# Performance work log

Hardware: AMD Instinct MI355X
Metric: run time of the kernel (lower is better)

Reference implementation:

```python
import jax, jax.numpy as jnp
import numpy as np
from jax import lax

N_CODES = 4880
T = 4096
VISIT_DIM = 512
HDIM = 512


def setup_inputs() -> dict:
    key = jax.random.key(0)
    ks = jax.random.split(key, 8)
    s_in = 1.0 / np.sqrt(HDIM)
    return {
        "H": jax.random.uniform(ks[0], (N_CODES, T), dtype=jnp.float32),
        "TE": jnp.zeros((1,), dtype=jnp.float32),
        "X_emb": jax.random.normal(ks[1], (N_CODES, VISIT_DIM), dtype=jnp.float32) * 0.02,
        "W_ih": jax.random.uniform(ks[2], (3 * HDIM, VISIT_DIM), minval=-s_in, maxval=s_in, dtype=jnp.float32),
        "W_hh": jax.random.uniform(ks[3], (3 * HDIM, HDIM), minval=-s_in, maxval=s_in, dtype=jnp.float32),
        "b_ih": jax.random.uniform(ks[4], (3 * HDIM,), minval=-s_in, maxval=s_in, dtype=jnp.float32),
        "b_hh": jax.random.uniform(ks[5], (3 * HDIM,), minval=-s_in, maxval=s_in, dtype=jnp.float32),
        "w_att": jax.random.uniform(ks[6], (1, HDIM), minval=-s_in, maxval=s_in, dtype=jnp.float32),
    }


def _gru_scan(visit_emb, W_ih, W_hh, b_ih, b_hh):
    # Precompute input projections for all timesteps: [T, 3H]
    gi = visit_emb @ W_ih.T + b_ih
    H = W_hh.shape[1]

    def step(h, gi_t):
        gh = h @ W_hh.T + b_hh  # [3H]
        i_r, i_z, i_n = gi_t[:H], gi_t[H:2 * H], gi_t[2 * H:]
        h_r, h_z, h_n = gh[:H], gh[H:2 * H], gh[2 * H:]
        r = jax.nn.sigmoid(i_r + h_r)
        z = jax.nn.sigmoid(i_z + h_z)
        n = jnp.tanh(i_n + r * h_n)
        h_new = (1.0 - z) * n + z * h
        return h_new, h_new

    h0 = jnp.zeros((H,), dtype=visit_emb.dtype)
    _, hs = lax.scan(step, h0, gi)
    return hs  # [T, H]


def reference(H, TE, X_emb, W_ih, W_hh, b_ih, b_hh, w_att):
    # visit embeddings: [T, visit_dim]
    visit_emb = H.T @ X_emb
    # GRU over the visit sequence (unbatched): [T, hdim]
    hidden_states = _gru_scan(visit_emb, W_ih, W_hh, b_ih, b_hh)
    # attention logits [T] -> softmax over visits
    logits = hidden_states @ w_att[0]
    alpha = jax.nn.softmax(logits)
    # diag(alpha) @ hidden summed over dim 0 == weighted sum over visits
    h = jnp.sum(alpha[:, None] * hidden_states, axis=0)  # [hdim]
    return h
```

## Files before the change

### kernel.cpp

```cpp
#include <hip/hip_runtime.h>

#define T_STEPS 4096
#define HD 512
#define G3HD 1536
#define NCODES 4880
#define NWG 16
#define SENT 0xFFFFFFFFu

typedef __attribute__((ext_vector_type(2))) float v2f;
typedef __attribute__((ext_vector_type(4))) unsigned uint4v;

__global__ __launch_bounds__(256) void gemm1_kernel(const float* __restrict__ H,
                                                    const float* __restrict__ X,
                                                    float* __restrict__ C) {
  __shared__ float As[16][68];
  __shared__ float Bs[16][68];
  const int m0 = blockIdx.x * 64;
  const int n0 = blockIdx.y * 64;
  const int tid = threadIdx.x;
  const int lk = tid >> 4;
  const int lm = (tid & 15) << 2;
  const int tm = (tid & 15) << 2;
  const int tn = (tid >> 4) << 2;
  float acc[4][4] = {};
  for (int k0 = 0; k0 < NCODES; k0 += 16) {
    float4 av = *(const float4*)(H + (size_t)(k0 + lk) * T_STEPS + m0 + lm);
    float4 bv = *(const float4*)(X + (size_t)(k0 + lk) * HD + n0 + lm);
    __syncthreads();
    *(float4*)(&As[lk][lm]) = av;
    *(float4*)(&Bs[lk][lm]) = bv;
    __syncthreads();
#pragma unroll
    for (int kk = 0; kk < 16; ++kk) {
      float4 a = *(const float4*)(&As[kk][tm]);
      float4 b = *(const float4*)(&Bs[kk][tn]);
      float ar[4] = {a.x, a.y, a.z, a.w};
      float br[4] = {b.x, b.y, b.z, b.w};
#pragma unroll
      for (int i = 0; i < 4; ++i)
#pragma unroll
        for (int j = 0; j < 4; ++j) acc[i][j] += ar[i] * br[j];
    }
  }
#pragma unroll
  for (int i = 0; i < 4; ++i) {
    float4 o = make_float4(acc[i][0], acc[i][1], acc[i][2], acc[i][3]);
    *(float4*)(C + (size_t)(m0 + tm + i) * HD + n0 + tn) = o;
  }
}

__global__ __launch_bounds__(256) void gemm2_kernel(const float* __restrict__ A,
                                                    const float* __restrict__ B,
                                                    const float* __restrict__ bias,
                                                    float* __restrict__ Cout) {
  __shared__ float As[16][68];
  __shared__ float Bs[16][68];
  const int m0 = blockIdx.x * 64;
  const int n0 = blockIdx.y * 64;
  const int tid = threadIdx.x;
  const int lr = tid >> 2;
  const int lkq = (tid & 3) << 2;
  const int tm = (tid & 15) << 2;
  const int tn = (tid >> 4) << 2;
  float acc[4][4] = {};
  for (int k0 = 0; k0 < HD; k0 += 16) {
    float4 av = *(const float4*)(A + (size_t)(m0 + lr) * HD + k0 + lkq);
    float4 bv = *(const float4*)(B + (size_t)(n0 + lr) * HD + k0 + lkq);
    __syncthreads();
    As[lkq + 0][lr] = av.x; As[lkq + 1][lr] = av.y;
    As[lkq + 2][lr] = av.z; As[lkq + 3][lr] = av.w;
    Bs[lkq + 0][lr] = bv.x; Bs[lkq + 1][lr] = bv.y;
    Bs[lkq + 2][lr] = bv.z; Bs[lkq + 3][lr] = bv.w;
    __syncthreads();
#pragma unroll
    for (int kk = 0; kk < 16; ++kk) {
      float4 a = *(const float4*)(&As[kk][tm]);
      float4 b = *(const float4*)(&Bs[kk][tn]);
      float ar[4] = {a.x, a.y, a.z, a.w};
      float br[4] = {b.x, b.y, b.z, b.w};
#pragma unroll
      for (int i = 0; i < 4; ++i)
#pragma unroll
        for (int j = 0; j < 4; ++j) acc[i][j] += ar[i] * br[j];
    }
  }
  const float b0 = bias[n0 + tn + 0];
  const float b1 = bias[n0 + tn + 1];
  const float b2 = bias[n0 + tn + 2];
  const float b3 = bias[n0 + tn + 3];
#pragma unroll
  for (int i = 0; i < 4; ++i) {
    float4 o = make_float4(acc[i][0] + b0, acc[i][1] + b1, acc[i][2] + b2, acc[i][3] + b3);
    *(float4*)(Cout + (size_t)(m0 + tm + i) * G3HD + n0 + tn) = o;
  }
}

__global__ __launch_bounds__(512, 1) void scan_kernel(const float* __restrict__ gi,
                                                      const float* __restrict__ W_hh,
                                                      const float* __restrict__ b_hh,
                                                      float* __restrict__ hs,
                                                      int* __restrict__ ctrl) {
  __shared__ int s_role;
  __shared__ __align__(16) float gibuf[2][64][96];
  __shared__ __align__(16) float hT[HD];
  __shared__ float part[8][3][32];
  const int tid = threadIdx.x;

  if (tid == 0) {
    int xcd;
    asm volatile("s_getreg_b32 %0, hwreg(HW_REG_XCC_ID)" : "=s"(xcd));
    int role = -1;
    const int slot = atomicAdd(&ctrl[xcd], 1);
    if (slot < NWG) {
      if (slot == NWG - 1) atomicCAS(&ctrl[8], -1, xcd);
      int wnr;
      while ((wnr = __hip_atomic_load(&ctrl[8], __ATOMIC_RELAXED,
                                      __HIP_MEMORY_SCOPE_AGENT)) < 0) {
        __builtin_amdgcn_s_sleep(16);
      }
      if (wnr == xcd) role = slot;
    }
    s_role = role;
  }
  __syncthreads();
  const int g = s_role;
  if (g < 0) return;

  const int w = tid >> 6;
  const int lane = tid & 63;
  const int e2 = lane & 31;
  const int q = lane >> 5;
  const int k0 = w * 64 + q * 32;

  v2f w2[3][16];
#pragma unroll
  for (int r = 0; r < 3; ++r) {
    const v2f* wp = (const v2f*)(W_hh + (size_t)(r * HD + g * 32 + e2) * HD + k0);
#pragma unroll
    for (int j = 0; j < 16; ++j) w2[r][j] = wp[j];
  }
#pragma unroll
  for (int r = 0; r < 3; ++r)
#pragma unroll
    for (int j = 0; j < 16; ++j) asm volatile("" : "+v"(w2[r][j]));

  float bh_r = 0.f, bh_z = 0.f, bh_n = 0.f, hprev = 0.f;
  if (tid < 32) {
    const int ej = g * 32 + tid;
    bh_r = b_hh[ej];
    bh_z = b_hh[HD + ej];
    bh_n = b_hh[2 * HD + ej];
  }

  unsigned* hs_u = (unsigned*)hs;

  uint4v st[3];
#pragma unroll
  for (int j = 0; j < 3; ++j) {
    const int c = tid + 512 * j, row = c / 24, seg = c % 24;
    st[j] = *(const uint4v*)(gi + (size_t)row * G3HD + (seg >> 3) * HD + g * 32 + (seg & 7) * 4);
  }
#pragma unroll
  for (int j = 0; j < 3; ++j) {
    const int c = tid + 512 * j, row = c / 24, seg = c % 24;
    *(uint4v*)&gibuf[0][row][(seg >> 3) * 32 + (seg & 7) * 4] = st[j];
  }
  __syncthreads();

  for (int t = 0; t < T_STEPS; ++t) {
    const int cb = (t >> 6) & 1;
    const int ts = t & 63;

    if (t == 0) {
      hT[tid] = 0.f;
    } else {
      const unsigned* hp = hs_u + (size_t)(t - 1) * HD + tid;
      unsigned v = __hip_atomic_load(hp, __ATOMIC_RELAXED, __HIP_MEMORY_SCOPE_AGENT);
      while (v == SENT)
        v = __hip_atomic_load(hp, __ATOMIC_RELAXED, __HIP_MEMORY_SCOPE_AGENT);
      hT[tid] = __uint_as_float(v);
    }
    __syncthreads();

    const v2f* hv = (const v2f*)&hT[k0];
    v2f h2[16];
#pragma unroll
    for (int m = 0; m < 16; ++m) h2[m] = hv[m];
    v2f a0 = (v2f)(0.f), a1 = (v2f)(0.f), a2 = (v2f)(0.f);
#pragma unroll
    for (int m = 0; m < 16; ++m) {
      a0 = __builtin_elementwise_fma(w2[0][m], h2[m], a0);
      a1 = __builtin_elementwise_fma(w2[1][m], h2[m], a1);
      a2 = __builtin_elementwise_fma(w2[2][m], h2[m], a2);
    }
    float s0 = a0.x + a0.y;
    float s1 = a1.x + a1.y;
    float s2 = a2.x + a2.y;
    s0 += __shfl_xor(s0, 32);
    s1 += __shfl_xor(s1, 32);
    s2 += __shfl_xor(s2, 32);
    if (q == 0) {
      part[w][0][e2] = s0;
      part[w][1][e2] = s1;
      part[w][2][e2] = s2;
    }

    if (ts == 0 && t + 64 < T_STEPS) {
#pragma unroll
      for (int j = 0; j < 3; ++j) {
        const int c = tid + 512 * j, row = c / 24, seg = c % 24;
        st[j] = *(const uint4v*)(gi + (size_t)(t + 64 + row) * G3HD + (seg >> 3) * HD +
                                 g * 32 + (seg & 7) * 4);
      }
    }
    if (ts == 1 && t + 63 < T_STEPS) {
#pragma unroll
      for (int j = 0; j < 3; ++j) {
        const int c = tid + 512 * j, row = c / 24, seg = c % 24;
        *(uint4v*)&gibuf[cb ^ 1][row][(seg >> 3) * 32 + (seg & 7) * 4] = st[j];
      }
    }
    __syncthreads();

    if (tid < 32) {
      float xr = 0.f, xz = 0.f, xn = 0.f;
#pragma unroll
      for (int ww = 0; ww < 8; ++ww) {
        xr += part[ww][0][tid];
        xz += part[ww][1][tid];
        xn += part[ww][2][tid];
      }
      const float gir = gibuf[cb][ts][tid];
      const float giz = gibuf[cb][ts][32 + tid];
      const float gin = gibuf[cb][ts][64 + tid];
      xr += gir + bh_r;
      xz += giz + bh_z;
      const float ghn = xn + bh_n;
      const float rr = __builtin_amdgcn_rcpf(1.f + __expf(-xr));
      const float zz = __builtin_amdgcn_rcpf(1.f + __expf(-xz));
      const float y = gin + rr * ghn;
      const float nn = 1.f - 2.f * __builtin_amdgcn_rcpf(__expf(2.f * y) + 1.f);
      const float hnew = nn + zz * (hprev - nn);
      __hip_atomic_store(hs_u + (size_t)t * HD + g * 32 + tid, __float_as_uint(hnew),
                         __ATOMIC_RELAXED, __HIP_MEMORY_SCOPE_AGENT);
      hprev = hnew;
    }
  }
}

__global__ __launch_bounds__(256) void logits_kernel(const float* __restrict__ hs,
                                                     const float* __restrict__ w_att,
                                                     float* __restrict__ logits) {
  const int tid = threadIdx.x;
  const int r = blockIdx.x * 32 + (tid >> 3);
  const int c0 = (tid & 7) * 64;
  const float4* hp = (const float4*)(hs + (size_t)r * HD + c0);
  const float4* wp = (const float4*)(w_att + c0);
  float acc = 0.f;
#pragma unroll
  for (int i = 0; i < 16; ++i) {
    float4 h4 = hp[i], w4 = wp[i];
    acc += h4.x * w4.x + h4.y * w4.y + h4.z * w4.z + h4.w * w4.w;
  }
  acc += __shfl_xor(acc, 1);
  acc += __shfl_xor(acc, 2);
  acc += __shfl_xor(acc, 4);
  if ((tid & 7) == 0) logits[r] = acc;
}

__global__ __launch_bounds__(256) void softmax_kernel(const float* __restrict__ logits,
                                                      float* __restrict__ alpha,
                                                      float* __restrict__ out) {
  __shared__ float tmp[4];
  const int tid = threadIdx.x;
  float l[16];
  float m = -1e30f;
#pragma unroll
  for (int i = 0; i < 16; ++i) {
    l[i] = logits[i * 256 + tid];
    m = fmaxf(m, l[i]);
  }
#pragma unroll
  for (int o = 32; o > 0; o >>= 1) m = fmaxf(m, __shfl_xor(m, o));
  if ((tid & 63) == 0) tmp[tid >> 6] = m;
  __syncthreads();
  m = fmaxf(fmaxf(tmp[0], tmp[1]), fmaxf(tmp[2], tmp[3]));
  __syncthreads();
  float e[16];
  float s = 0.f;
#pragma unroll
  for (int i = 0; i < 16; ++i) {
    e[i] = expf(l[i] - m);
    s += e[i];
  }
#pragma unroll
  for (int o = 32; o > 0; o >>= 1) s += __shfl_xor(s, o);
  if ((tid & 63) == 0) tmp[tid >> 6] = s;
  __syncthreads();
  s = tmp[0] + tmp[1] + tmp[2] + tmp[3];
  const float inv = 1.f / s;
#pragma unroll
  for (int i = 0; i < 16; ++i) alpha[i * 256 + tid] = e[i] * inv;
  out[tid] = 0.f;
  out[256 + tid] = 0.f;
}

__global__ __launch_bounds__(256) void wsum_kernel(const float* __restrict__ alpha,
                                                   const float* __restrict__ hs,
                                                   float* __restrict__ out) {
  const int tid = threadIdx.x;
  const int jblk = (blockIdx.x & 1) * 256;
  const int tc = blockIdx.x >> 1;
  float acc = 0.f;
  for (int tt = 0; tt < 64; ++tt) {
    const int t = tc * 64 + tt;
    acc += alpha[t] * hs[(size_t)t * HD + jblk + tid];
  }
  atomicAdd(&out[jblk + tid], acc);
}

extern "C" void kernel_launch(void* const* d_in, const int* in_sizes, int n_in,
                              void* d_out, int out_size, void* d_ws, size_t ws_size,
                              hipStream_t stream) {
  const float* H     = (const float*)d_in[0];
  const float* X_emb = (const float*)d_in[2];
  const float* W_ih  = (const float*)d_in[3];
  const float* W_hh  = (const float*)d_in[4];
  const float* b_ih  = (const float*)d_in[5];
  const float* b_hh  = (const float*)d_in[6];
  const float* w_att = (const float*)d_in[7];
  float* out = (float*)d_out;

  char* ws = (char*)d_ws;
  float* visit  = (float*)(ws + 0);
  float* gi     = (float*)(ws + 8388608);
  float* hs     = (float*)(ws + 33554432);
  float* logits = (float*)(ws + 41943040);
  float* alpha  = (float*)(ws + 41959424);
  int*   ctrl   = (int*)(ws + 41975808);

  hipMemsetAsync(hs, 0xFF, (size_t)T_STEPS * HD * sizeof(float), stream);
  hipMemsetAsync(ctrl, 0, 8 * sizeof(int), stream);
  hipMemsetAsync(ctrl + 8, 0xFF, sizeof(int), stream);

  gemm1_kernel<<<dim3(64, 8), 256, 0, stream>>>(H, X_emb, visit);
  gemm2_kernel<<<dim3(64, 24), 256, 0, stream>>>(visit, W_ih, b_ih, gi);
  scan_kernel<<<256, 512, 0, stream>>>(gi, W_hh, b_hh, hs, ctrl);
  logits_kernel<<<128, 256, 0, stream>>>(hs, w_att, logits);
  softmax_kernel<<<1, 256, 0, stream>>>(logits, alpha, out);
  wsum_kernel<<<128, 256, 0, stream>>>(alpha, hs, out);
}
```

Measured before the change: 5.558 ms.

## Remap GRU scan threads so reductions stay in-wave, drop one barrier per step

Changes the scan kernel's work split so each wave owns 4 output elements and 16 lanes split the K dimension of each. The dot products are reduced with in-wave xor shuffles, which removes the shared-memory partial buffer and the second __syncthreads per timestep. The h vector is double-buffered in LDS so the next step's write cannot race with reads, and a rotated access pattern is used to avoid bank conflicts. Gate math now runs on 32 lanes spread over 8 waves instead of one wave, at the cost of extra shuffle steps.

```diff
diff --git a/kernel.cpp b/kernel.cpp
--- a/kernel.cpp
+++ b/kernel.cpp
@@ -102,8 +102,7 @@
                                                       int* __restrict__ ctrl) {
   __shared__ int s_role;
   __shared__ __align__(16) float gibuf[2][64][96];
-  __shared__ __align__(16) float hT[HD];
-  __shared__ float part[8][3][32];
+  __shared__ __align__(16) float hT[2][HD];
   const int tid = threadIdx.x;
 
   if (tid == 0) {
@@ -128,120 +127,111 @@
 
   const int w = tid >> 6;
   const int lane = tid & 63;
-  const int e2 = lane & 31;
-  const int q = lane >> 5;
-  const int k0 = w * 64 + q * 32;
+  const int kk = lane & 15;
+  const int j = lane >> 4;
+  const int eg = g * 32 + w * 4 + j;
 
   v2f w2[3][16];
 #pragma unroll
   for (int r = 0; r < 3; ++r) {
-    const v2f* wp = (const v2f*)(W_hh + (size_t)(r * HD + g * 32 + e2) * HD + k0);
-#pragma unroll
-    for (int j = 0; j < 16; ++j) w2[r][j] = wp[j];
+    const v2f* wp = (const v2f*)(W_hh + (size_t)(r * HD + eg) * HD + kk * 32);
+#pragma unroll
+    for (int s = 0; s < 16; ++s) w2[r][s] = wp[(s + kk) & 15];
   }
 #pragma unroll
   for (int r = 0; r < 3; ++r)
 #pragma unroll
-    for (int j = 0; j < 16; ++j) asm volatile("" : "+v"(w2[r][j]));
-
+    for (int s = 0; s < 16; ++s) asm volatile("" : "+v"(w2[r][s]));
+
+  const bool is_gate = (kk == 0);
   float bh_r = 0.f, bh_z = 0.f, bh_n = 0.f, hprev = 0.f;
-  if (tid < 32) {
-    const int ej = g * 32 + tid;
-    bh_r = b_hh[ej];
-    bh_z = b_hh[HD + ej];
-    bh_n = b_hh[2 * HD + ej];
+  if (is_gate) {
+    bh_r = b_hh[eg];
+    bh_z = b_hh[HD + eg];
+    bh_n = b_hh[2 * HD + eg];
   }
 
   unsigned* hs_u = (unsigned*)hs;
 
   uint4v st[3];
 #pragma unroll
-  for (int j = 0; j < 3; ++j) {
-    const int c = tid + 512 * j, row = c / 24, seg = c % 24;
-    st[j] = *(const uint4v*)(gi + (size_t)row * G3HD + (seg >> 3) * HD + g * 32 + (seg & 7) * 4);
-  }
-#pragma unroll
-  for (int j = 0; j < 3; ++j) {
-    const int c = tid + 512 * j, row = c / 24, seg = c % 24;
-    *(uint4v*)&gibuf[0][row][(seg >> 3) * 32 + (seg & 7) * 4] = st[j];
+  for (int jj = 0; jj < 3; ++jj) {
+    const int c = tid + 512 * jj, row = c / 24, seg = c % 24;
+    st[jj] = *(const uint4v*)(gi + (size_t)row * G3HD + (seg >> 3) * HD + g * 32 + (seg & 7) * 4);
+  }
+#pragma unroll
+  for (int jj = 0; jj < 3; ++jj) {
+    const int c = tid + 512 * jj, row = c / 24, seg = c % 24;
+    *(uint4v*)&gibuf[0][row][(seg >> 3) * 32 + (seg & 7) * 4] = st[jj];
   }
   __syncthreads();
 
   for (int t = 0; t < T_STEPS; ++t) {
+    const int pb = t & 1;
     const int cb = (t >> 6) & 1;
     const int ts = t & 63;
 
     if (t == 0) {
-      hT[tid] = 0.f;
+      hT[0][tid] = 0.f;
     } else {
       const unsigned* hp = hs_u + (size_t)(t - 1) * HD + tid;
       unsigned v = __hip_atomic_load(hp, __ATOMIC_RELAXED, __HIP_MEMORY_SCOPE_AGENT);
       while (v == SENT)
         v = __hip_atomic_load(hp, __ATOMIC_RELAXED, __HIP_MEMORY_SCOPE_AGENT);
-      hT[tid] = __uint_as_float(v);
-    }
-    __syncthreads();
-
-    const v2f* hv = (const v2f*)&hT[k0];
+      hT[pb][tid] = __uint_as_float(v);
+    }
+
+    if (ts == 0 && t + 64 < T_STEPS) {
+#pragma unroll
+      for (int jj = 0; jj < 3; ++jj) {
+        const int c = tid + 512 * jj, row = c / 24, seg = c % 24;
+        st[jj] = *(const uint4v*)(gi + (size_t)(t + 64 + row) * G3HD + (seg >> 3) * HD +
+                                 g * 32 + (seg & 7) * 4);
+      }
+    }
+    __syncthreads();
+
+    if (ts == 1 && t + 63 < T_STEPS) {
+#pragma unroll
+      for (int jj = 0; jj < 3; ++jj) {
+        const int c = tid + 512 * jj, row = c / 24, seg = c % 24;
+        *(uint4v*)&gibuf[cb ^ 1][row][(seg >> 3) * 32 + (seg & 7) * 4] = st[jj];
+      }
+    }
+
+    const v2f* hv = (const v2f*)&hT[pb][kk * 32];
     v2f h2[16];
 #pragma unroll
-    for (int m = 0; m < 16; ++m) h2[m] = hv[m];
+    for (int s = 0; s < 16; ++s) h2[s] = hv[(s + kk) & 15];
     v2f a0 = (v2f)(0.f), a1 = (v2f)(0.f), a2 = (v2f)(0.f);
 #pragma unroll
-    for (int m = 0; m < 16; ++m) {
-      a0 = __builtin_elementwise_fma(w2[0][m], h2[m], a0);
-      a1 = __builtin_elementwise_fma(w2[1][m], h2[m], a1);
-      a2 = __builtin_elementwise_fma(w2[2][m], h2[m], a2);
+    for (int s = 0; s < 16; ++s) {
+      a0 = __builtin_elementwise_fma(w2[0][s], h2[s], a0);
+      a1 = __builtin_elementwise_fma(w2[1][s], h2[s], a1);
+      a2 = __builtin_elementwise_fma(w2[2][s], h2[s], a2);
     }
     float s0 = a0.x + a0.y;
     float s1 = a1.x + a1.y;
     float s2 = a2.x + a2.y;
-    s0 += __shfl_xor(s0, 32);
-    s1 += __shfl_xor(s1, 32);
-    s2 += __shfl_xor(s2, 32);
-    if (q == 0) {
-      part[w][0][e2] = s0;
-      part[w][1][e2] = s1;
-      part[w][2][e2] = s2;
-    }
-
-    if (ts == 0 && t + 64 < T_STEPS) {
-#pragma unroll
-      for (int j = 0; j < 3; ++j) {
-        const int c = tid + 512 * j, row = c / 24, seg = c % 24;
-        st[j] = *(const uint4v*)(gi + (size_t)(t + 64 + row) * G3HD + (seg >> 3) * HD +
-                                 g * 32 + (seg & 7) * 4);
-      }
-    }
-    if (ts == 1 && t + 63 < T_STEPS) {
-#pragma unroll
-      for (int j = 0; j < 3; ++j) {
-        const int c = tid + 512 * j, row = c / 24, seg = c % 24;
-        *(uint4v*)&gibuf[cb ^ 1][row][(seg >> 3) * 32 + (seg & 7) * 4] = st[j];
-      }
-    }
-    __syncthreads();
-
-    if (tid < 32) {
-      float xr = 0.f, xz = 0.f, xn = 0.f;
-#pragma unroll
-      for (int ww = 0; ww < 8; ++ww) {
-        xr += part[ww][0][tid];
-        xz += part[ww][1][tid];
-        xn += part[ww][2][tid];
-      }
-      const float gir = gibuf[cb][ts][tid];
-      const float giz = gibuf[cb][ts][32 + tid];
-      const float gin = gibuf[cb][ts][64 + tid];
-      xr += gir + bh_r;
-      xz += giz + bh_z;
-      const float ghn = xn + bh_n;
+#pragma unroll
+    for (int mask = 1; mask <= 8; mask <<= 1) {
+      s0 += __shfl_xor(s0, mask);
+      s1 += __shfl_xor(s1, mask);
+      s2 += __shfl_xor(s2, mask);
+    }
+
+    if (is_gate) {
+      const int el = w * 4 + j;
+      float xr = s0 + gibuf[cb][ts][el] + bh_r;
+      float xz = s1 + gibuf[cb][ts][32 + el] + bh_z;
+      const float ghn = s2 + bh_n;
+      const float gin = gibuf[cb][ts][64 + el];
       const float rr = __builtin_amdgcn_rcpf(1.f + __expf(-xr));
       const float zz = __builtin_amdgcn_rcpf(1.f + __expf(-xz));
       const float y = gin + rr * ghn;
       const float nn = 1.f - 2.f * __builtin_amdgcn_rcpf(__expf(2.f * y) + 1.f);
       const float hnew = nn + zz * (hprev - nn);
-      __hip_atomic_store(hs_u + (size_t)t * HD + g * 32 + tid, __float_as_uint(hnew),
+      __hip_atomic_store(hs_u + (size_t)t * HD + eg, __float_as_uint(hnew),
                          __ATOMIC_RELAXED, __HIP_MEMORY_SCOPE_AGENT);
       hprev = hnew;
     }
```

Measured after the change: 8.669 ms. 56.0% more time.

## Poll previous hidden state directly into registers, dropping the per-step LDS barrier

Applied to the files above, without the earlier changes.

Each half-wave now spin-loads its own 32-element slice of the previous hidden state from global memory with vectorized sc1 loads straight into registers. This removes the shared hT staging buffer and one __syncthreads per timestep. The partial-sum buffer is double-buffered by step parity so the single remaining barrier still keeps reads and writes separate. In exchange, polling traffic per step rises (each lane reads 128 bytes instead of 4) and correctness now depends on the inline-asm cache-bypass semantics.

```diff
diff --git a/kernel.cpp b/kernel.cpp
--- a/kernel.cpp
+++ b/kernel.cpp
@@ -102,8 +102,7 @@
                                                       int* __restrict__ ctrl) {
   __shared__ int s_role;
   __shared__ __align__(16) float gibuf[2][64][96];
-  __shared__ __align__(16) float hT[HD];
-  __shared__ float part[8][3][32];
+  __shared__ float part[2][8][3][32];
   const int tid = threadIdx.x;
 
   if (tid == 0) {
@@ -131,6 +130,7 @@
   const int e2 = lane & 31;
   const int q = lane >> 5;
   const int k0 = w * 64 + q * 32;
+  const int c = 2 * w + q;
 
   v2f w2[3][16];
 #pragma unroll
@@ -157,35 +157,71 @@
   uint4v st[3];
 #pragma unroll
   for (int j = 0; j < 3; ++j) {
-    const int c = tid + 512 * j, row = c / 24, seg = c % 24;
+    const int cc = tid + 512 * j, row = cc / 24, seg = cc % 24;
     st[j] = *(const uint4v*)(gi + (size_t)row * G3HD + (seg >> 3) * HD + g * 32 + (seg & 7) * 4);
   }
 #pragma unroll
   for (int j = 0; j < 3; ++j) {
-    const int c = tid + 512 * j, row = c / 24, seg = c % 24;
+    const int cc = tid + 512 * j, row = cc / 24, seg = cc % 24;
     *(uint4v*)&gibuf[0][row][(seg >> 3) * 32 + (seg & 7) * 4] = st[j];
   }
   __syncthreads();
 
   for (int t = 0; t < T_STEPS; ++t) {
+    const int pb = t & 1;
     const int cb = (t >> 6) & 1;
     const int ts = t & 63;
 
+    v2f h2[16];
     if (t == 0) {
-      hT[tid] = 0.f;
+#pragma unroll
+      for (int m = 0; m < 16; ++m) h2[m] = (v2f)(0.f);
     } else {
-      const unsigned* hp = hs_u + (size_t)(t - 1) * HD + tid;
-      unsigned v = __hip_atomic_load(hp, __ATOMIC_RELAXED, __HIP_MEMORY_SCOPE_AGENT);
-      while (v == SENT)
-        v = __hip_atomic_load(hp, __ATOMIC_RELAXED, __HIP_MEMORY_SCOPE_AGENT);
-      hT[tid] = __uint_as_float(v);
-    }
-    __syncthreads();
-
-    const v2f* hv = (const v2f*)&hT[k0];
-    v2f h2[16];
-#pragma unroll
-    for (int m = 0; m < 16; ++m) h2[m] = hv[m];
+      const unsigned* hp = hs_u + (size_t)(t - 1) * HD + c * 32;
+      uint4v b0, b1, b2, b3, b4, b5, b6, b7;
+      bool ok;
+      do {
+        asm volatile(
+            "global_load_dwordx4 %0, %8, off sc1\n\t"
+            "global_load_dwordx4 %1, %8, off offset:16 sc1\n\t"
+            "global_load_dwordx4 %2, %8, off offset:32 sc1\n\t"
+            "global_load_dwordx4 %3, %8, off offset:48 sc1\n\t"
+            "global_load_dwordx4 %4, %8, off offset:64 sc1\n\t"
+            "global_load_dwordx4 %5, %8, off offset:80 sc1\n\t"
+            "global_load_dwordx4 %6, %8, off offset:96 sc1\n\t"
+            "global_load_dwordx4 %7, %8, off offset:112 sc1\n\t"
+            "s_waitcnt vmcnt(0)"
+            : "=&v"(b0), "=&v"(b1), "=&v"(b2), "=&v"(b3),
+              "=&v"(b4), "=&v"(b5), "=&v"(b6), "=&v"(b7)
+            : "v"(hp)
+            : "memory");
+        ok = (b0.x != SENT) & (b0.y != SENT) & (b0.z != SENT) & (b0.w != SENT) &
+             (b1.x != SENT) & (b1.y != SENT) & (b1.z != SENT) & (b1.w != SENT) &
+             (b2.x != SENT) & (b2.y != SENT) & (b2.z != SENT) & (b2.w != SENT) &
+             (b3.x != SENT) & (b3.y != SENT) & (b3.z != SENT) & (b3.w != SENT) &
+             (b4.x != SENT) & (b4.y != SENT) & (b4.z != SENT) & (b4.w != SENT) &
+             (b5.x != SENT) & (b5.y != SENT) & (b5.z != SENT) & (b5.w != SENT) &
+             (b6.x != SENT) & (b6.y != SENT) & (b6.z != SENT) & (b6.w != SENT) &
+             (b7.x != SENT) & (b7.y != SENT) & (b7.z != SENT) & (b7.w != SENT);
+      } while (!ok);
+      h2[0].x  = __uint_as_float(b0.x); h2[0].y  = __uint_as_float(b0.y);
+      h2[1].x  = __uint_as_float(b0.z); h2[1].y  = __uint_as_float(b0.w);
+      h2[2].x  = __uint_as_float(b1.x); h2[2].y  = __uint_as_float(b1.y);
+      h2[3].x  = __uint_as_float(b1.z); h2[3].y  = __uint_as_float(b1.w);
+      h2[4].x  = __uint_as_float(b2.x); h2[4].y  = __uint_as_float(b2.y);
+      h2[5].x  = __uint_as_float(b2.z); h2[5].y  = __uint_as_float(b2.w);
+      h2[6].x  = __uint_as_float(b3.x); h2[6].y  = __uint_as_float(b3.y);
+      h2[7].x  = __uint_as_float(b3.z); h2[7].y  = __uint_as_float(b3.w);
+      h2[8].x  = __uint_as_float(b4.x); h2[8].y  = __uint_as_float(b4.y);
+      h2[9].x  = __uint_as_float(b4.z); h2[9].y  = __uint_as_float(b4.w);
+      h2[10].x = __uint_as_float(b5.x); h2[10].y = __uint_as_float(b5.y);
+      h2[11].x = __uint_as_float(b5.z); h2[11].y = __uint_as_float(b5.w);
+      h2[12].x = __uint_as_float(b6.x); h2[12].y = __uint_as_float(b6.y);
+      h2[13].x = __uint_as_float(b6.z); h2[13].y = __uint_as_float(b6.w);
+      h2[14].x = __uint_as_float(b7.x); h2[14].y = __uint_as_float(b7.y);
+      h2[15].x = __uint_as_float(b7.z); h2[15].y = __uint_as_float(b7.w);
+    }
+
     v2f a0 = (v2f)(0.f), a1 = (v2f)(0.f), a2 = (v2f)(0.f);
 #pragma unroll
     for (int m = 0; m < 16; ++m) {
@@ -200,15 +236,15 @@
     s1 += __shfl_xor(s1, 32);
     s2 += __shfl_xor(s2, 32);
     if (q == 0) {
-      part[w][0][e2] = s0;
-      part[w][1][e2] = s1;
-      part[w][2][e2] = s2;
+      part[pb][w][0][e2] = s0;
+      part[pb][w][1][e2] = s1;
+      part[pb][w][2][e2] = s2;
     }
 
     if (ts == 0 && t + 64 < T_STEPS) {
 #pragma unroll
       for (int j = 0; j < 3; ++j) {
-        const int c = tid + 512 * j, row = c / 24, seg = c % 24;
+        const int cc = tid + 512 * j, row = cc / 24, seg = cc % 24;
         st[j] = *(const uint4v*)(gi + (size_t)(t + 64 + row) * G3HD + (seg >> 3) * HD +
                                  g * 32 + (seg & 7) * 4);
       }
@@ -216,7 +252,7 @@
     if (ts == 1 && t + 63 < T_STEPS) {
 #pragma unroll
       for (int j = 0; j < 3; ++j) {
-        const int c = tid + 512 * j, row = c / 24, seg = c % 24;
+        const int cc = tid + 512 * j, row = cc / 24, seg = cc % 24;
         *(uint4v*)&gibuf[cb ^ 1][row][(seg >> 3) * 32 + (seg & 7) * 4] = st[j];
       }
     }
@@ -226,9 +262,9 @@
       float xr = 0.f, xz = 0.f, xn = 0.f;
 #pragma unroll
       for (int ww = 0; ww < 8; ++ww) {
-        xr += part[ww][0][tid];
-        xz += part[ww][1][tid];
-        xn += part[ww][2][tid];
+        xr += part[pb][ww][0][tid];
+        xz += part[pb][ww][1][tid];
+        xn += part[pb][ww][2][tid];
       }
       const float gir = gibuf[cb][ts][tid];
       const float giz = gibuf[cb][ts][32 + tid];
```

Result: slower. 9.338 ms (+68.0%).
